# Optimization experiments

Measured on AMD Instinct MI355X. Metric: run time of the kernel, lower is better.

The kernel has to match this reference:

```python
import jax, jax.numpy as jnp
import numpy as np

NEUMANN_TERMS = 6
EPS_PASSTHROUGH = 1e-6  # hn_config.GRADIENT_PASSTHROUGH_EPSILON (assumed)


def _cayley_neumann(W, terms=NEUMANN_TERMS):
    """Cayley transform U = (I - A)^{-1} (I + A) with A = skew(W),
    where (I - A)^{-1} is approximated by the truncated Neumann series
    sum_{k=0}^{terms-1} A^k."""
    A = 0.5 * (W - W.T)                       # skew-symmetric generator
    I = jnp.eye(W.shape[0], dtype=W.dtype)
    S = I
    P = I
    for _ in range(terms - 1):                # small fixed loop (neumann_terms)
        P = P @ A
        S = S + P
    return S @ (I + A)


def _quantum_rotation(h, theta):
    """Parametric quantum rotation activation: rotate adjacent feature pairs
    by angle theta (norm-preserving, replaces ReLU/GELU)."""
    N, d = h.shape
    hp = h.reshape(N, d // 2, 2)
    c, s = jnp.cos(theta), jnp.sin(theta)
    x0, x1 = hp[..., 0], hp[..., 1]
    r0 = c * x0 - s * x1
    r1 = s * x0 + c * x1
    return jnp.stack([r0, r1], axis=-1).reshape(N, d)


def setup_inputs() -> dict:
    key = jax.random.key(0)
    k1, k2, k3 = jax.random.split(key, 3)
    N, d_model, d_ff = 65536, 1024, 1024
    inputs = jax.random.normal(k1, (N, d_model), dtype=jnp.float32)
    # Orthogonal initializer with gain 0.1 (as in build())
    q1 = jnp.linalg.qr(jax.random.normal(k2, (d_ff, d_model), dtype=jnp.float32))[0]
    q2 = jnp.linalg.qr(jax.random.normal(k3, (d_model, d_ff), dtype=jnp.float32))[0]
    u1_weights = 0.1 * q1
    u2_weights = 0.1 * q2
    activation_angle = jnp.float32(0.7854)  # pi/4 initializer
    return {"inputs": inputs, "u1_weights": u1_weights,
            "u2_weights": u2_weights, "activation_angle": activation_angle}


def reference(inputs, u1_weights, u2_weights, activation_angle):
    U1 = _cayley_neumann(u1_weights)          # [d_ff, d_model]
    U2 = _cayley_neumann(u2_weights)          # [d_model, d_ff]
    h = inputs @ U1.T                         # [N, d_ff]
    h = _quantum_rotation(h, activation_angle)
    out = h @ U2.T                            # [N, d_model]
    # gradient passthrough term from call()
    passthrough = (jnp.mean(u1_weights) * EPS_PASSTHROUGH
                   + jnp.mean(u2_weights) * EPS_PASSTHROUGH
                   + activation_angle * EPS_PASSTHROUGH)
    return out + passthrough
```

## Files before the change

### kernel.cpp

```cpp
#include <hip/hip_runtime.h>
#include <hip/hip_bf16.h>
#include <stdint.h>


#define MM (1024 * 1024)

typedef __attribute__((ext_vector_type(4))) float f32x4;
typedef __attribute__((ext_vector_type(8))) short bf16x8;

__device__ __forceinline__ ushort f2bf(float f) {
  uint32_t u = __builtin_bit_cast(uint32_t, f);
  u += 0x7FFFu + ((u >> 16) & 1u);
  return (ushort)(u >> 16);
}
__device__ __forceinline__ float bf2f(ushort h) {
  uint32_t u = ((uint32_t)h) << 16;
  return __builtin_bit_cast(float, u);
}

__device__ __forceinline__ void gld_lds16(const ushort* g, ushort* l) {
  __builtin_amdgcn_global_load_lds(
      (const __attribute__((address_space(1))) unsigned int*)g,
      (__attribute__((address_space(3))) unsigned int*)l, 16, 0, 0);
}

#define STAGE(GS, LB, BUF, H, KT)                                      \
  do {                                                                 \
    const ushort* g_ = (GS) + (size_t)((H)*128) * K + (size_t)(KT)*64; \
    ushort* d_ = (LB) + (BUF)*32768 + (H)*128 * 64;                    \
    gld_lds16(g_, d_);                                                 \
    gld_lds16(g_ + (size_t)64 * K, d_ + 64 * 64);                      \
  } while (0)

#define LDA(MH, BUF)                                                        \
  do {                                                                      \
    _Pragma("unroll") for (int ti = 0; ti < 4; ++ti) {                      \
      const ushort* p_ = rdA + (BUF)*32768 + ((MH)*64 + ti * 16 + lr) * 64; \
      af[ti][0] = *(const bf16x8*)(p_ + (pcol0 >> 1));                      \
      af[ti][1] = *(const bf16x8*)(p_ + (pcol1 >> 1));                      \
    }                                                                       \
  } while (0)

#define LDB(NH, BUF)                                                        \
  do {                                                                      \
    _Pragma("unroll") for (int tj = 0; tj < 2; ++tj) {                      \
      const ushort* p_ = rdB + (BUF)*32768 + ((NH)*32 + tj * 16 + lr) * 64; \
      bfr[tj][0] = *(const bf16x8*)(p_ + (pcol0 >> 1));                     \
      bfr[tj][1] = *(const bf16x8*)(p_ + (pcol1 >> 1));                     \
    }                                                                       \
  } while (0)

#define MFMA16(MH, NH)                                                  \
  do {                                                                  \
    __builtin_amdgcn_s_setprio(1);                                      \
    _Pragma("unroll") for (int m_ = 0; m_ < 4; ++m_)                    \
    _Pragma("unroll") for (int n_ = 0; n_ < 2; ++n_)                    \
    _Pragma("unroll") for (int ks_ = 0; ks_ < 2; ++ks_)                 \
      acc[(MH)*4 + m_][(NH)*2 + n_] =                                   \
          __builtin_amdgcn_mfma_f32_16x16x32_bf16(                      \
              af[m_][ks_], bfr[n_][ks_], acc[(MH)*4 + m_][(NH)*2 + n_], \
              0, 0, 0);                                                 \
    __builtin_amdgcn_s_setprio(0);                                      \
  } while (0)

#define CFENCE asm volatile("" ::: "memory")
#define SBAR                           \
  do {                                 \
    CFENCE;                            \
    __builtin_amdgcn_s_barrier();      \
    __builtin_amdgcn_sched_barrier(0); \
  } while (0)

__global__ __launch_bounds__(512, 2) void gemm256(
    const ushort* __restrict__ X, const ushort* __restrict__ Y,
    float* __restrict__ o32, ushort* __restrict__ o16, int M, int N, int K,
    int mode, const float* __restrict__ theta_p,
    const float* __restrict__ sums) {
  extern __shared__ ushort lds[];

  const int tid = threadIdx.x;
  const int wave = tid >> 6, lane = tid & 63;

  const int nwg = gridDim.x * gridDim.y;
  const int lin = blockIdx.y * gridDim.x + blockIdx.x;
  const int wgid = (lin & 7) * (nwg >> 3) + (lin >> 3);
  const int bn = wgid & 3;
  const int bm = wgid >> 2;

  const int wrow = wave >> 2;
  const int wcol = wave & 3;

  const int srow = wave * 8 + (lane >> 3);
  const int scol = (((lane & 7) ^ ((lane >> 3) & 7)) << 3);
  const ushort* Xs = X + (size_t)(bm * 256 + srow) * K + scol;
  const ushort* Ys = Y + (size_t)(bn * 256 + srow) * K + scol;
  ushort* stA = lds + wave * 8 * 64;
  ushort* stB = lds + 16384 + wave * 8 * 64;

  const int lr = lane & 15;
  const int kqb = (lane >> 4) << 4;
  const int swz = (lr & 7) << 4;
  const int pcol0 = (0 + kqb) ^ swz;
  const int pcol1 = (64 + kqb) ^ swz;
  const ushort* rdA = lds + wrow * 128 * 64;
  const ushort* rdB = lds + 16384 + wcol * 64 * 64;

  f32x4 acc[8][4] = {};
  bf16x8 af[4][2], bfr[2][2];

  const int NT = K >> 6;

  STAGE(Xs, stA, 0, 0, 0);
  STAGE(Xs, stA, 0, 1, 0);
  STAGE(Ys, stB, 0, 0, 0);
  STAGE(Ys, stB, 0, 1, 0);

  for (int t = 0; t < NT; ++t) {
    const int cur = t & 1, nxt = cur ^ 1;
    if (t + 1 < NT) {
      STAGE(Xs, stA, nxt, 0, t + 1);
      STAGE(Xs, stA, nxt, 1, t + 1);
      STAGE(Ys, stB, nxt, 0, t + 1);
      STAGE(Ys, stB, nxt, 1, t + 1);
      asm volatile("s_waitcnt vmcnt(8)" ::: "memory");
    } else {
      asm volatile("s_waitcnt vmcnt(0)" ::: "memory");
    }
    SBAR;
    LDA(0, cur);
    LDB(0, cur);
    MFMA16(0, 0);
    SBAR;
    LDB(1, cur);
    SBAR;
    MFMA16(0, 1);
    SBAR;
    LDA(1, cur);
    SBAR;
    MFMA16(1, 1);
    SBAR;
    LDB(0, cur);
    SBAR;
    MFMA16(1, 0);
    SBAR;
  }

  const int q4 = (lane >> 4) * 4;
  const int rbase = bm * 256 + wrow * 128;
  const int cbase = bn * 256 + wcol * 64;
  if (mode == 1) {
    float th = *theta_p, s, c;
    __sincosf(th, &s, &c);
    const float ssgn = (lane & 1) ? s : -s;
#pragma unroll
    for (int fi = 0; fi < 8; ++fi)
#pragma unroll
      for (int r = 0; r < 4; ++r) {
        const size_t row = (size_t)(rbase + fi * 16 + q4 + r);
        ushort* Orow = o16 + row * N;
#pragma unroll
        for (int fj = 0; fj < 4; ++fj) {
          float v = acc[fi][fj][r];
          float w = __shfl_xor(v, 1);
          Orow[cbase + fj * 16 + lr] = f2bf(c * v + ssgn * w);
        }
      }
  } else {
    const float pt = 1e-6f * (sums[0] * (1.0f / 1048576.0f) +
                              sums[1] * (1.0f / 1048576.0f) + *theta_p);
#pragma unroll
    for (int fi = 0; fi < 8; ++fi)
#pragma unroll
      for (int r = 0; r < 4; ++r) {
        const size_t row = (size_t)(rbase + fi * 16 + q4 + r);
        float* Orow = o32 + row * N;
#pragma unroll
        for (int fj = 0; fj < 4; ++fj)
          Orow[cbase + fj * 16 + lr] = acc[fi][fj][r] + pt;
      }
  }
}

__global__ __launch_bounds__(256, 2) void gemm_bt(
    const ushort* __restrict__ X0, const ushort* __restrict__ Y0,
    float* __restrict__ o32, ushort* __restrict__ o16,
    ushort* __restrict__ o16b, const float* __restrict__ auxf,
    const ushort* __restrict__ auxb, int M, int N, int K, int mode,
    const float* __restrict__ theta_p, const float* __restrict__ sums) {
  __shared__ ushort lA[128 * 32];
  __shared__ ushort lB[128 * 32];

  const int tid = threadIdx.x;
  const int wave = tid >> 6, lane = tid & 63;
  const int mi = blockIdx.z & 1;

  const int nwg = gridDim.x * gridDim.y;
  const int lin = blockIdx.y * gridDim.x + blockIdx.x;
  const int swzb = (lin & 7) * (nwg >> 3) + (lin >> 3);
  const int bn = swzb & 7;
  const int bm = swzb >> 3;

  const ushort* X = X0 + (size_t)mi * MM;
  const ushort* Y = Y0 + (size_t)mi * MM;

  const ushort* Xg = X + (size_t)(bm * 128 + (tid >> 2)) * K + (tid & 3) * 8;
  const ushort* Yg = Y + (size_t)(bn * 128 + (tid >> 2)) * K + (tid & 3) * 8;
  ushort* lAw = lA + wave * 512;
  ushort* lBw = lB + wave * 512;

  const int wm = (wave & 1) * 64;
  const int wn = (wave >> 1) * 64;
  const int lr = lane & 15;
  const int kq = (lane >> 4) * 8;

  f32x4 acc[4][4] = {};

  for (int k0 = 0; k0 < K; k0 += 32) {
    __syncthreads();
    gld_lds16(Xg + k0, lAw);
    gld_lds16(Xg + k0 + (size_t)64 * K, lAw + 64 * 32);
    gld_lds16(Yg + k0, lBw);
    gld_lds16(Yg + k0 + (size_t)64 * K, lBw + 64 * 32);
    __syncthreads();

    bf16x8 afv[4], bfg[4];
#pragma unroll
    for (int t = 0; t < 4; ++t) {
      afv[t] = *(const bf16x8*)(lA + (wm + t * 16 + lr) * 32 + kq);
      bfg[t] = *(const bf16x8*)(lB + (wn + t * 16 + lr) * 32 + kq);
    }
#pragma unroll
    for (int ti = 0; ti < 4; ++ti)
#pragma unroll
      for (int tj = 0; tj < 4; ++tj)
        acc[ti][tj] = __builtin_amdgcn_mfma_f32_16x16x32_bf16(
            afv[ti], bfg[tj], acc[ti][tj], 0, 0, 0);
  }

  const int q4 = (lane >> 4) * 4;
  const size_t zoff = (size_t)mi * MM;
  float* O = (mode == 3) ? o32 + zoff : nullptr;
  ushort* P0 = o16 + zoff;
  ushort* P1 = (mode == 3) ? o16b + zoff : nullptr;
  const float* Ax = (mode == 4) ? auxf + zoff : nullptr;
  const ushort* Ab = (mode == 3) ? auxb + zoff : nullptr;
#pragma unroll
  for (int ti = 0; ti < 4; ++ti)
#pragma unroll
    for (int r = 0; r < 4; ++r) {
      const int row = bm * 128 + wm + ti * 16 + q4 + r;
      const size_t base = (size_t)row * N;
#pragma unroll
      for (int tj = 0; tj < 4; ++tj) {
        const int col = bn * 128 + wn + tj * 16 + lr;
        const float v = acc[ti][tj][r];
        const float diag = (row == col) ? 1.f : 0.f;
        if (mode == 3) {
          O[base + col] = v;
          P0[base + col] = f2bf(-v);
          P1[base + col] = f2bf(diag + 2.f * bf2f(Ab[base + col]) - v);
        } else if (mode == 4) {
          P0[base + col] = f2bf(diag - Ax[base + col] + v);
        } else {
          P0[base + col] = f2bf(v);
        }
      }
    }
}

__global__ __launch_bounds__(256) void prep_a(const float* __restrict__ W1,
                                              const float* __restrict__ W2,
                                              ushort* __restrict__ Abf,
                                              float* __restrict__ sums) {
  __shared__ float sT[32][33];
  const int z = blockIdx.z;
  const float* W = z ? W2 : W1;
  ushort* A = Abf + (size_t)z * MM;
  const int r0 = blockIdx.y * 32, c0 = blockIdx.x * 32;
  const int x = threadIdx.x, y = threadIdx.y;

#pragma unroll
  for (int k = 0; k < 4; ++k)
    sT[y + 8 * k][x] = W[(size_t)(c0 + y + 8 * k) * 1024 + r0 + x];
  __syncthreads();

  float lsum = 0.f;
#pragma unroll
  for (int k = 0; k < 4; ++k) {
    int i = y + 8 * k;
    float w = W[(size_t)(r0 + i) * 1024 + c0 + x];
    lsum += w;
    A[(size_t)(r0 + i) * 1024 + c0 + x] = f2bf(0.5f * (w - sT[x][i]));
  }
#pragma unroll
  for (int off = 32; off > 0; off >>= 1) lsum += __shfl_down(lsum, off);
  if (((y * 32 + x) & 63) == 0) atomicAdd(&sums[z], lsum);
}

__global__ __launch_bounds__(256) void cvt_x(const float* __restrict__ x,
                                             ushort* __restrict__ xb) {
  const size_t i = (size_t)blockIdx.x * 256 + threadIdx.x;
  float4 v = ((const float4*)x)[i];
  ushort4 o;
  o.x = f2bf(v.x);
  o.y = f2bf(v.y);
  o.z = f2bf(v.z);
  o.w = f2bf(v.w);
  ((ushort4*)xb)[i] = o;
}

extern "C" void kernel_launch(void* const* d_in, const int* in_sizes, int n_in,
                              void* d_out, int out_size, void* d_ws,
                              size_t ws_size, hipStream_t stream) {
  const float* xin = (const float*)d_in[0];
  const float* w1 = (const float*)d_in[1];
  const float* w2 = (const float*)d_in[2];
  const float* th = (const float*)d_in[3];
  float* out = (float*)d_out;

  char* w = (char*)d_ws;
  float* sums = (float*)w;
  ushort* Abf = (ushort*)(w + 256);
  ushort* Bbf = Abf + 2 * MM;
  ushort* Gbf = Bbf + 2 * MM;
  ushort* Fbf = Gbf + 2 * MM;
  ushort* Ubf = Fbf + 2 * MM;
  float* S1 = (float*)(Ubf + 2 * MM);
  ushort* xbf = (ushort*)(S1 + 2 * MM);
  ushort* hbf = xbf + (size_t)65536 * 1024;

  static bool inited = false;
  if (!inited) {
    (void)hipFuncSetAttribute((const void*)gemm256,
                              hipFuncAttributeMaxDynamicSharedMemorySize,
                              131072);
    inited = true;
  }

  hipMemsetAsync(sums, 0, 2 * sizeof(float), stream);

  prep_a<<<dim3(32, 32, 2), dim3(32, 8), 0, stream>>>(w1, w2, Abf, sums);
  cvt_x<<<65536, 256, 0, stream>>>(xin, xbf);

  gemm_bt<<<dim3(8, 8, 2), 256, 0, stream>>>(Abf, Abf, S1, Bbf, Gbf, nullptr,
                                             Abf, 1024, 1024, 1024, 3, th,
                                             sums);
  gemm_bt<<<dim3(8, 8, 2), 256, 0, stream>>>(Bbf, Bbf, nullptr, Fbf, nullptr,
                                             S1, nullptr, 1024, 1024, 1024, 4,
                                             th, sums);
  gemm_bt<<<dim3(8, 8, 2), 256, 0, stream>>>(Gbf, Fbf, nullptr, Ubf, nullptr,
                                             nullptr, nullptr, 1024, 1024,
                                             1024, 5, th, sums);

  gemm256<<<dim3(4, 256, 1), 512, 131072, stream>>>(
      xbf, Ubf, nullptr, hbf, 65536, 1024, 1024, 1, th, sums);
  gemm256<<<dim3(4, 256, 1), 512, 131072, stream>>>(
      hbf, Ubf + MM, out, nullptr, 65536, 1024, 1024, 2, th, sums);
}
```

Measured before the change: 959.4 us.

## Restructure big GEMM main loop to triple-buffered K=32 tiles with one barrier

The main GEMM kernel moves from a double-buffered K=64 tile loop with eight barriers per step to a triple-buffered K=32 tile loop with a single barrier per step. Each wave loads all A and B fragments and then issues 32 MFMAs, with the next-next tile prefetched via direct global-to-LDS loads. The XOR swizzle on LDS rows is dropped and LDS use falls from 128KB to 96KB. Unswizzled 64-byte rows may cause LDS bank conflicts, and the shorter K step gives less MFMA work per barrier.

```diff
diff --git a/kernel.cpp b/kernel.cpp
--- a/kernel.cpp
+++ b/kernel.cpp
@@ -24,51 +24,19 @@
       (__attribute__((address_space(3))) unsigned int*)l, 16, 0, 0);
 }
 
-#define STAGE(GS, LB, BUF, H, KT)                                      \
-  do {                                                                 \
-    const ushort* g_ = (GS) + (size_t)((H)*128) * K + (size_t)(KT)*64; \
-    ushort* d_ = (LB) + (BUF)*32768 + (H)*128 * 64;                    \
-    gld_lds16(g_, d_);                                                 \
-    gld_lds16(g_ + (size_t)64 * K, d_ + 64 * 64);                      \
-  } while (0)
-
-#define LDA(MH, BUF)                                                        \
-  do {                                                                      \
-    _Pragma("unroll") for (int ti = 0; ti < 4; ++ti) {                      \
-      const ushort* p_ = rdA + (BUF)*32768 + ((MH)*64 + ti * 16 + lr) * 64; \
-      af[ti][0] = *(const bf16x8*)(p_ + (pcol0 >> 1));                      \
-      af[ti][1] = *(const bf16x8*)(p_ + (pcol1 >> 1));                      \
-    }                                                                       \
-  } while (0)
-
-#define LDB(NH, BUF)                                                        \
-  do {                                                                      \
-    _Pragma("unroll") for (int tj = 0; tj < 2; ++tj) {                      \
-      const ushort* p_ = rdB + (BUF)*32768 + ((NH)*32 + tj * 16 + lr) * 64; \
-      bfr[tj][0] = *(const bf16x8*)(p_ + (pcol0 >> 1));                     \
-      bfr[tj][1] = *(const bf16x8*)(p_ + (pcol1 >> 1));                     \
-    }                                                                       \
-  } while (0)
-
-#define MFMA16(MH, NH)                                                  \
-  do {                                                                  \
-    __builtin_amdgcn_s_setprio(1);                                      \
-    _Pragma("unroll") for (int m_ = 0; m_ < 4; ++m_)                    \
-    _Pragma("unroll") for (int n_ = 0; n_ < 2; ++n_)                    \
-    _Pragma("unroll") for (int ks_ = 0; ks_ < 2; ++ks_)                 \
-      acc[(MH)*4 + m_][(NH)*2 + n_] =                                   \
-          __builtin_amdgcn_mfma_f32_16x16x32_bf16(                      \
-              af[m_][ks_], bfr[n_][ks_], acc[(MH)*4 + m_][(NH)*2 + n_], \
-              0, 0, 0);                                                 \
-    __builtin_amdgcn_s_setprio(0);                                      \
-  } while (0)
-
-#define CFENCE asm volatile("" ::: "memory")
 #define SBAR                           \
   do {                                 \
-    CFENCE;                            \
+    asm volatile("" ::: "memory");     \
     __builtin_amdgcn_s_barrier();      \
     __builtin_amdgcn_sched_barrier(0); \
+  } while (0)
+
+#define STAGE4(BO, KT)                                             \
+  do {                                                             \
+    gld_lds16(Xs + (KT)*32, stW + (BO));                           \
+    gld_lds16(Xs + (KT)*32 + (size_t)128 * K, stW + (BO) + 4096);  \
+    gld_lds16(Ys + (KT)*32, stW + (BO) + 8192);                    \
+    gld_lds16(Ys + (KT)*32 + (size_t)128 * K, stW + (BO) + 12288); \
   } while (0)
 
 __global__ __launch_bounds__(512, 2) void gemm256(
@@ -89,60 +57,54 @@
 
   const int wrow = wave >> 2;
   const int wcol = wave & 3;
-
-  const int srow = wave * 8 + (lane >> 3);
-  const int scol = (((lane & 7) ^ ((lane >> 3) & 7)) << 3);
-  const ushort* Xs = X + (size_t)(bm * 256 + srow) * K + scol;
-  const ushort* Ys = Y + (size_t)(bn * 256 + srow) * K + scol;
-  ushort* stA = lds + wave * 8 * 64;
-  ushort* stB = lds + 16384 + wave * 8 * 64;
-
   const int lr = lane & 15;
-  const int kqb = (lane >> 4) << 4;
-  const int swz = (lr & 7) << 4;
-  const int pcol0 = (0 + kqb) ^ swz;
-  const int pcol1 = (64 + kqb) ^ swz;
-  const ushort* rdA = lds + wrow * 128 * 64;
-  const ushort* rdB = lds + 16384 + wcol * 64 * 64;
+  const int kq = (lane >> 4) * 8;
+
+  const ushort* Xs = X + (size_t)(bm * 256 + (tid >> 2)) * K + (tid & 3) * 8;
+  const ushort* Ys = Y + (size_t)(bn * 256 + (tid >> 2)) * K + (tid & 3) * 8;
+  ushort* stW = lds + wave * 512;
+
+  const ushort* rdA = lds + (wrow * 128 + lr) * 32 + kq;
+  const ushort* rdB = lds + 8192 + (wcol * 64 + lr) * 32 + kq;
 
   f32x4 acc[8][4] = {};
-  bf16x8 af[4][2], bfr[2][2];
-
-  const int NT = K >> 6;
-
-  STAGE(Xs, stA, 0, 0, 0);
-  STAGE(Xs, stA, 0, 1, 0);
-  STAGE(Ys, stB, 0, 0, 0);
-  STAGE(Ys, stB, 0, 1, 0);
+
+  const int NT = K >> 5;
+  int cb = 0;
+  int sb = 2 * 16384;
+
+  STAGE4(0, 0);
+  STAGE4(16384, 1);
+  asm volatile("s_waitcnt vmcnt(4)" ::: "memory");
 
   for (int t = 0; t < NT; ++t) {
-    const int cur = t & 1, nxt = cur ^ 1;
-    if (t + 1 < NT) {
-      STAGE(Xs, stA, nxt, 0, t + 1);
-      STAGE(Xs, stA, nxt, 1, t + 1);
-      STAGE(Ys, stB, nxt, 0, t + 1);
-      STAGE(Ys, stB, nxt, 1, t + 1);
-      asm volatile("s_waitcnt vmcnt(8)" ::: "memory");
-    } else {
+    SBAR;
+    if (t + 2 < NT) STAGE4(sb, t + 2);
+
+    bf16x8 af[8], bv[4];
+#pragma unroll
+    for (int ti = 0; ti < 8; ++ti)
+      af[ti] = *(const bf16x8*)(rdA + cb + ti * (16 * 32));
+#pragma unroll
+    for (int tj = 0; tj < 4; ++tj)
+      bv[tj] = *(const bf16x8*)(rdB + cb + tj * (16 * 32));
+
+    __builtin_amdgcn_s_setprio(1);
+#pragma unroll
+    for (int ti = 0; ti < 8; ++ti)
+#pragma unroll
+      for (int tj = 0; tj < 4; ++tj)
+        acc[ti][tj] = __builtin_amdgcn_mfma_f32_16x16x32_bf16(
+            af[ti], bv[tj], acc[ti][tj], 0, 0, 0);
+    __builtin_amdgcn_s_setprio(0);
+
+    if (t + 2 < NT)
+      asm volatile("s_waitcnt vmcnt(4)" ::: "memory");
+    else if (t + 1 < NT)
       asm volatile("s_waitcnt vmcnt(0)" ::: "memory");
-    }
-    SBAR;
-    LDA(0, cur);
-    LDB(0, cur);
-    MFMA16(0, 0);
-    SBAR;
-    LDB(1, cur);
-    SBAR;
-    MFMA16(0, 1);
-    SBAR;
-    LDA(1, cur);
-    SBAR;
-    MFMA16(1, 1);
-    SBAR;
-    LDB(0, cur);
-    SBAR;
-    MFMA16(1, 0);
-    SBAR;
+
+    cb = (cb == 2 * 16384) ? 0 : cb + 16384;
+    sb = (sb == 2 * 16384) ? 0 : sb + 16384;
   }
 
   const int q4 = (lane >> 4) * 4;
@@ -333,7 +295,7 @@
   if (!inited) {
     (void)hipFuncSetAttribute((const void*)gemm256,
                               hipFuncAttributeMaxDynamicSharedMemorySize,
-                              131072);
+                              98304);
     inited = true;
   }
 
@@ -352,8 +314,8 @@
                                              nullptr, nullptr, 1024, 1024,
                                              1024, 5, th, sums);
 
-  gemm256<<<dim3(4, 256, 1), 512, 131072, stream>>>(
+  gemm256<<<dim3(4, 256, 1), 512, 98304, stream>>>(
       xbf, Ubf, nullptr, hbf, 65536, 1024, 1024, 1, th, sums);
-  gemm256<<<dim3(4, 256, 1), 512, 131072, stream>>>(
+  gemm256<<<dim3(4, 256, 1), 512, 98304, stream>>>(
       hbf, Ubf + MM, out, nullptr, 65536, 1024, 1024, 2, th, sums);
 }
```

New measurement: 932.1 us. 1.03x faster.
